# Performance work log

Hardware: AMD Instinct MI355X
Metric: run time of the kernel (lower is better)

## Reference

```python
import jax, jax.numpy as jnp
import numpy as np

NUM_EMBEDDINGS = 1024
EMBEDDING_DIM = 64
COMMITMENT_COST = 0.25
EPSILON = 1e-10


def setup_inputs() -> dict:
    key = jax.random.key(0)
    k1, k2 = jax.random.split(key)
    z_e = jax.random.normal(k1, (32, EMBEDDING_DIM, 64, 64), dtype=jnp.float32)
    # torch init: uniform(-1/K, 1/K)
    lim = 1.0 / NUM_EMBEDDINGS
    embedding = jax.random.uniform(k2, (NUM_EMBEDDINGS, EMBEDDING_DIM),
                                   dtype=jnp.float32, minval=-lim, maxval=lim)
    return {"z_e": z_e, "embedding": embedding}


def reference(z_e, embedding):
    # NCHW -> NHWC
    z = jnp.transpose(z_e, (0, 2, 3, 1))  # [B,H,W,D]
    input_shape = z.shape
    flat = z.reshape(-1, EMBEDDING_DIM)  # [N,D]

    x2 = jnp.sum(flat ** 2, axis=1, keepdims=True)          # [N,1]
    e2 = jnp.sum(embedding ** 2, axis=1)                     # [K]
    ip = jnp.matmul(flat, embedding.T)                       # [N,K]
    distances = x2 + e2 - 2.0 * ip

    encoding_indices = jnp.argmin(distances, axis=1)         # [N]
    encodings = jax.nn.one_hot(encoding_indices, NUM_EMBEDDINGS,
                               dtype=jnp.float32)            # [N,K]

    z_q = jnp.matmul(encodings, embedding).reshape(input_shape)  # [B,H,W,D]

    commitment_loss = COMMITMENT_COST * jnp.mean((jax.lax.stop_gradient(z_q) - z) ** 2)
    e2z_loss = jnp.mean((z_q - jax.lax.stop_gradient(z)) ** 2)
    vq_loss = commitment_loss + e2z_loss

    # straight-through estimator
    z_q = z + jax.lax.stop_gradient(z_q - z)

    avg_probs = jnp.mean(encodings, axis=0)  # [K]
    perplexity = jnp.exp(-jnp.sum(avg_probs * jnp.log(avg_probs + EPSILON)))

    z_q_out = jnp.transpose(z_q, (0, 3, 1, 2))  # back to NCHW
    return (vq_loss, z_q_out, perplexity, encodings)
```

## Files before the change

### kernel.cpp

```cpp
#include <hip/hip_runtime.h>
#include <cfloat>
#include <stdint.h>


typedef __attribute__((ext_vector_type(8))) short bf8v;
typedef __attribute__((ext_vector_type(4))) float f4v;

__device__ __forceinline__ unsigned short f2bf(float v) {
  unsigned u = __float_as_uint(v);
  return (unsigned short)((u + 0x7FFFu + ((u >> 16) & 1u)) >> 16);
}
__device__ __forceinline__ float bf2f(unsigned short h) {
  return __uint_as_float(((unsigned)h) << 16);
}

__global__ __launch_bounds__(256) void vq_prep(const float* __restrict__ emb,
                                               float* __restrict__ ws) {
  #pragma clang fp contract(off)
  int gid = blockIdx.x * 256 + threadIdx.x;
  if (gid == 0) ws[0] = 0.0f;
  ((int*)ws)[1 + gid] = 0;
  const float* e = emb + (gid << 6);
  float r[8];
  #pragma unroll
  for (int j = 0; j < 8; ++j) r[j] = e[j] * e[j];
  #pragma unroll
  for (int i = 8; i < 64; i += 8) {
    #pragma unroll
    for (int j = 0; j < 8; ++j) { float s = e[i + j] * e[i + j]; r[j] = r[j] + s; }
  }
  ws[1025 + gid] = ((r[0] + r[1]) + (r[2] + r[3])) + ((r[4] + r[5]) + (r[6] + r[7]));
}

__global__ __launch_bounds__(256) void vq_prep_frags(const float* __restrict__ emb,
                                                     float* __restrict__ out) {
  int e = blockIdx.x * 256 + threadIdx.x;
  int lane = e & 63, sub = e >> 6;
  int term = sub % 3, kk = (sub / 3) & 1, nt = sub / 6;
  int code = nt * 16 + (lane & 15);
  int d0 = kk * 32 + (lane >> 4) * 8;
  const float* src = emb + code * 64 + d0;
  unsigned short hs[8];
  #pragma unroll
  for (int j = 0; j < 8; ++j) {
    float v = src[j];
    unsigned short h = f2bf(v);  float r1 = v - bf2f(h);
    unsigned short m = f2bf(r1); float r2 = r1 - bf2f(m);
    unsigned short l = f2bf(r2);
    hs[j] = (term == 0) ? h : (term == 1) ? m : l;
  }
  uint4 p;
  p.x = (unsigned)hs[0] | ((unsigned)hs[1] << 16);
  p.y = (unsigned)hs[2] | ((unsigned)hs[3] << 16);
  p.z = (unsigned)hs[4] | ((unsigned)hs[5] << 16);
  p.w = (unsigned)hs[6] | ((unsigned)hs[7] << 16);
  ((uint4*)(out + 4))[e] = p;
}

__global__ __launch_bounds__(256, 4) void vq_main(const float* __restrict__ ze,
                                                  float* __restrict__ ws,
                                                  float* __restrict__ out) {
  __shared__ float xtile[64 * 68];
  __shared__ __align__(16) short bbuf[2 * 6 * 64 * 8];
  __shared__ float e2s[1024];
  __shared__ float x2s[64];
  __shared__ float sx[256];

  int t = threadIdx.x;
  int w = __builtin_amdgcn_readfirstlane(t >> 6);
  int lane = t & 63;
  int g = blockIdx.x;
  int b = g >> 6, h = g & 63;
  int n0 = g << 6;

  const float* zebase = ze + ((size_t)b << 18) + (h << 6);
  #pragma unroll
  for (int i = 0; i < 16; ++i) {
    int d = w * 16 + i;
    xtile[lane * 68 + d] = zebase[d * 4096 + lane];
  }
  e2s[t] = ws[1025 + t];         e2s[256 + t] = ws[1281 + t];
  e2s[512 + t] = ws[1537 + t];   e2s[768 + t] = ws[1793 + t];
  __syncthreads();

  {
    #pragma clang fp contract(off)
    const float* xr = xtile + lane * 68;
    int j0 = 2 * w, j1 = 2 * w + 1;
    float v0 = xr[j0], v1 = xr[j1];
    float ra = v0 * v0, rb = v1 * v1;
    #pragma unroll
    for (int p = 1; p < 8; ++p) {
      float s0 = xr[8 * p + j0]; s0 = s0 * s0; ra = ra + s0;
      float s1 = xr[8 * p + j1]; s1 = s1 * s1; rb = rb + s1;
    }
    sx[lane * 4 + w] = ra + rb;
  }
  __syncthreads();
  if (t < 64) x2s[t] = (sx[t * 4] + sx[t * 4 + 1]) + (sx[t * 4 + 2] + sx[t * 4 + 3]);
  __syncthreads();

  int qd = lane >> 4, rr = lane & 15;
  const float* xr = xtile + (w * 16 + rr) * 68;
  bf8v Ah[2], Am[2], Al[2];
  #pragma unroll
  for (int kk = 0; kk < 2; ++kk) {
    #pragma unroll
    for (int j = 0; j < 8; ++j) {
      float v = xr[kk * 32 + qd * 8 + j];
      unsigned short hh = f2bf(v);  float r1 = v - bf2f(hh);
      unsigned short mm = f2bf(r1); float r2 = r1 - bf2f(mm);
      unsigned short ll = f2bf(r2);
      Ah[kk][j] = (short)hh; Am[kk][j] = (short)mm; Al[kk][j] = (short)ll;
    }
  }
  float x2v[4];
  #pragma unroll
  for (int r = 0; r < 4; ++r) x2v[r] = x2s[w * 16 + qd * 4 + r];

  const uint4* ft = (const uint4*)(out + 4);
  uint4* bput = (uint4*)bbuf;
  float* encbase = out + 8388610 + (size_t)n0 * 1024;
  const float2 z2 = make_float2(0.0f, 0.0f);

  for (int f = w; f < 6; f += 4) bput[f * 64 + lane] = ft[f * 64 + lane];
  __syncthreads();

  unsigned long long best[4] = {~0ULL, ~0ULL, ~0ULL, ~0ULL};

  #pragma unroll 1
  for (int nt = 0; nt < 64; ++nt) {
    int cur = nt & 1, nxt = cur ^ 1;
    uint4 pv0, pv1;
    if (nt < 63) {
      pv0 = ft[((nt + 1) * 6 + w) * 64 + lane];
      if (w < 2) pv1 = ft[((nt + 1) * 6 + w + 4) * 64 + lane];
    }
    float e2v = e2s[nt * 16 + (lane & 15)];
    f4v acc = {0.0f, 0.0f, 0.0f, 0.0f};
    const bf8v* bb = (const bf8v*)bbuf + cur * 6 * 64;
    #pragma unroll
    for (int kk = 0; kk < 2; ++kk) {
      bf8v Bh = bb[(kk * 3 + 0) * 64 + lane];
      bf8v Bm = bb[(kk * 3 + 1) * 64 + lane];
      bf8v Bl = bb[(kk * 3 + 2) * 64 + lane];
      acc = __builtin_amdgcn_mfma_f32_16x16x32_bf16(Ah[kk], Bh, acc, 0, 0, 0);
      acc = __builtin_amdgcn_mfma_f32_16x16x32_bf16(Ah[kk], Bm, acc, 0, 0, 0);
      acc = __builtin_amdgcn_mfma_f32_16x16x32_bf16(Am[kk], Bh, acc, 0, 0, 0);
      acc = __builtin_amdgcn_mfma_f32_16x16x32_bf16(Am[kk], Bm, acc, 0, 0, 0);
      acc = __builtin_amdgcn_mfma_f32_16x16x32_bf16(Ah[kk], Bl, acc, 0, 0, 0);
      acc = __builtin_amdgcn_mfma_f32_16x16x32_bf16(Al[kk], Bh, acc, 0, 0, 0);
    }
    unsigned code0 = (unsigned)(nt * 16 + (lane & 15));
    #pragma unroll
    for (int r = 0; r < 4; ++r) {
      float tt = x2v[r] + e2v;
      float dd = fmaf(-2.0f, acc[r], tt);
      unsigned long long cand =
          (((unsigned long long)__float_as_uint(dd)) << 32) | code0;
      if (cand < best[r]) best[r] = cand;
    }
    float2* ez = (float2*)(encbase + nt * 1024) + t;
    ez[0] = z2; ez[256] = z2;
    if (nt < 63) {
      bput[(nxt * 6 + w) * 64 + lane] = pv0;
      if (w < 2) bput[(nxt * 6 + w + 4) * 64 + lane] = pv1;
    }
    __syncthreads();
  }

  #pragma unroll
  for (int r = 0; r < 4; ++r) {
    unsigned long long bu = best[r];
    #pragma unroll
    for (int m = 1; m <= 8; m <<= 1) {
      unsigned long long o = __shfl_xor(bu, m, 64);
      if (o < bu) bu = o;
    }
    best[r] = bu;
  }
  if ((lane & 15) == 0) {
    #pragma unroll
    for (int r = 0; r < 4; ++r)
      ((int*)encbase)[w * 16 + qd * 4 + r] = (int)(best[r] & 0xFFFFFFFFu);
  }
}

__global__ __launch_bounds__(256) void vq_out(const float* __restrict__ ze,
                                              const float* __restrict__ emb,
                                              float* __restrict__ ws,
                                              float* __restrict__ out) {
  __shared__ float red[4];
  int g = blockIdx.x, t = threadIdx.x;
  int b = g >> 6, h = g & 63, n0 = g << 6;
  float* enc = out + 8388610;
  int* wp = (int*)(enc + (size_t)n0 * 1024);
  int row = t & 63;
  int gi = wp[row];
  __syncthreads();
  if (t < 64) ((float*)wp)[t] = 0.0f;
  __syncthreads();
  if (t < 64) enc[(size_t)(n0 + t) * 1024 + gi] = 1.0f;

  const float* er = emb + gi * 64;
  const float* zr = ze + ((size_t)b << 18) + (h << 6) + row;
  float* qr = out + 1 + ((size_t)b << 18) + (h << 6) + row;
  float ls = 0.0f;
  #pragma unroll
  for (int i = 0; i < 16; ++i) {
    int d = (t >> 6) * 16 + i;
    float v = er[d];
    float df = v - zr[(size_t)d * 4096];
    ls = fmaf(df, df, ls);
    qr[(size_t)d * 4096] = v;
  }
  #pragma unroll
  for (int off = 32; off > 0; off >>= 1) ls += __shfl_down(ls, off, 64);
  if ((t & 63) == 0) red[t >> 6] = ls;
  __syncthreads();
  if (t == 0) atomicAdd(ws, (red[0] + red[1]) + (red[2] + red[3]));
  if (t < 64) atomicAdd((int*)ws + 1 + gi, 1);
}

__global__ __launch_bounds__(1024) void vq_fin(const float* __restrict__ ws,
                                               float* __restrict__ out) {
  __shared__ float sm[16];
  int t = threadIdx.x;
  const int* counts = (const int*)ws + 1;
  float c = (float)counts[t];
  float p = c * (1.0f / 131072.0f);
  float s = p * logf(p + 1e-10f);
  #pragma unroll
  for (int off = 32; off > 0; off >>= 1) s += __shfl_down(s, off, 64);
  if ((t & 63) == 0) sm[t >> 6] = s;
  __syncthreads();
  if (t == 0) {
    float v = 0.0f;
    #pragma unroll
    for (int i = 0; i < 16; ++i) v += sm[i];
    out[8388609] = expf(-v);
    float m = ws[0] / 8388608.0f;
    out[0] = 0.25f * m + m;
  }
}

extern "C" void kernel_launch(void* const* d_in, const int* in_sizes, int n_in,
                              void* d_out, int out_size, void* d_ws, size_t ws_size,
                              hipStream_t stream) {
  const float* ze  = (const float*)d_in[0];
  const float* emb = (const float*)d_in[1];
  float* out = (float*)d_out;
  float* ws  = (float*)d_ws;
  vq_prep<<<4, 256, 0, stream>>>(emb, ws);
  vq_prep_frags<<<96, 256, 0, stream>>>(emb, out);
  vq_main<<<2048, 256, 0, stream>>>(ze, ws, out);
  vq_out<<<2048, 256, 0, stream>>>(ze, emb, ws, out);
  vq_fin<<<1, 1024, 0, stream>>>(ws, out);
}
```

Measured before the change: 664.9 us.

## Move encoding zero-fill to output kernel and derive loss from min distance

The zeroing of the 512 MB one-hot encodings buffer moves out of the MFMA distance loop into vq_out, so the compute loop no longer carries heavy global stores. The loss is now the sum of the selected minimum distances, accumulated with an atomic in vq_main, and vq_out no longer reads z_e. Code-usage histogram atomics also move into vq_main. The distance-based loss relies on the expanded ||x||^2+||e||^2-2x.e form, which can differ slightly from the direct squared difference because of cancellation.

```diff
diff --git a/kernel.cpp b/kernel.cpp
--- a/kernel.cpp
+++ b/kernel.cpp
@@ -121,7 +121,6 @@
   const uint4* ft = (const uint4*)(out + 4);
   uint4* bput = (uint4*)bbuf;
   float* encbase = out + 8388610 + (size_t)n0 * 1024;
-  const float2 z2 = make_float2(0.0f, 0.0f);
 
   for (int f = w; f < 6; f += 4) bput[f * 64 + lane] = ft[f * 64 + lane];
   __syncthreads();
@@ -160,8 +159,6 @@
           (((unsigned long long)__float_as_uint(dd)) << 32) | code0;
       if (cand < best[r]) best[r] = cand;
     }
-    float2* ez = (float2*)(encbase + nt * 1024) + t;
-    ez[0] = z2; ez[256] = z2;
     if (nt < 63) {
       bput[(nxt * 6 + w) * 64 + lane] = pv0;
       if (w < 2) bput[(nxt * 6 + w + 4) * 64 + lane] = pv1;
@@ -179,47 +176,50 @@
     }
     best[r] = bu;
   }
+
+  float s4 = 0.0f;
+  #pragma unroll
+  for (int r = 0; r < 4; ++r) s4 += __uint_as_float((unsigned)(best[r] >> 32));
+  s4 += __shfl_xor(s4, 16, 64);
+  s4 += __shfl_xor(s4, 32, 64);
+  if (lane == 0) atomicAdd(ws, s4);
   if ((lane & 15) == 0) {
     #pragma unroll
-    for (int r = 0; r < 4; ++r)
-      ((int*)encbase)[w * 16 + qd * 4 + r] = (int)(best[r] & 0xFFFFFFFFu);
-  }
-}
-
-__global__ __launch_bounds__(256) void vq_out(const float* __restrict__ ze,
-                                              const float* __restrict__ emb,
-                                              float* __restrict__ ws,
+    for (int r = 0; r < 4; ++r) {
+      int code = (int)(best[r] & 0xFFFFFFFFu);
+      ((int*)encbase)[w * 16 + qd * 4 + r] = code;
+      atomicAdd((int*)ws + 1 + code, 1);
+    }
+  }
+}
+
+__global__ __launch_bounds__(256) void vq_out(const float* __restrict__ emb,
                                               float* __restrict__ out) {
-  __shared__ float red[4];
+  __shared__ int swin[64];
   int g = blockIdx.x, t = threadIdx.x;
   int b = g >> 6, h = g & 63, n0 = g << 6;
   float* enc = out + 8388610;
-  int* wp = (int*)(enc + (size_t)n0 * 1024);
+  float* encb = enc + (size_t)n0 * 1024;
+  if (t < 64) swin[t] = ((int*)encb)[t];
+  __syncthreads();
+
+  const float2 z2 = make_float2(0.0f, 0.0f);
+  float2* ez = (float2*)encb;
+  #pragma unroll 8
+  for (int i = 0; i < 256; ++i) ez[i * 256 + t] = z2;
+  __syncthreads();
+
   int row = t & 63;
-  int gi = wp[row];
-  __syncthreads();
-  if (t < 64) ((float*)wp)[t] = 0.0f;
-  __syncthreads();
-  if (t < 64) enc[(size_t)(n0 + t) * 1024 + gi] = 1.0f;
+  int gi = swin[row];
+  if (t < 64) enc[(size_t)(n0 + t) * 1024 + swin[t]] = 1.0f;
 
   const float* er = emb + gi * 64;
-  const float* zr = ze + ((size_t)b << 18) + (h << 6) + row;
   float* qr = out + 1 + ((size_t)b << 18) + (h << 6) + row;
-  float ls = 0.0f;
   #pragma unroll
   for (int i = 0; i < 16; ++i) {
     int d = (t >> 6) * 16 + i;
-    float v = er[d];
-    float df = v - zr[(size_t)d * 4096];
-    ls = fmaf(df, df, ls);
-    qr[(size_t)d * 4096] = v;
-  }
-  #pragma unroll
-  for (int off = 32; off > 0; off >>= 1) ls += __shfl_down(ls, off, 64);
-  if ((t & 63) == 0) red[t >> 6] = ls;
-  __syncthreads();
-  if (t == 0) atomicAdd(ws, (red[0] + red[1]) + (red[2] + red[3]));
-  if (t < 64) atomicAdd((int*)ws + 1 + gi, 1);
+    qr[(size_t)d * 4096] = er[d];
+  }
 }
 
 __global__ __launch_bounds__(1024) void vq_fin(const float* __restrict__ ws,
@@ -254,6 +254,6 @@
   vq_prep<<<4, 256, 0, stream>>>(emb, ws);
   vq_prep_frags<<<96, 256, 0, stream>>>(emb, out);
   vq_main<<<2048, 256, 0, stream>>>(ze, ws, out);
-  vq_out<<<2048, 256, 0, stream>>>(ze, emb, ws, out);
+  vq_out<<<2048, 256, 0, stream>>>(emb, out);
   vq_fin<<<1, 1024, 0, stream>>>(ws, out);
 }
```

New measurement: 817.0 us. 1.23x slower.
